# Kernel optimization log

Hardware: AMD Instinct MI355X
Metric: run time of the kernel (lower is better)

The kernel has to match this reference:

```python
import jax, jax.numpy as jnp
import numpy as np


def setup_inputs() -> dict:
    key = jax.random.key(0)
    k1, k2 = jax.random.split(key)
    P, N, D = 8, 4096, 1024
    LOAD = 16384
    data = jax.random.normal(k1, (P, N, D), dtype=jnp.float32)
    tags = jax.random.randint(k2, (P, N), 0, LOAD, dtype=jnp.int64)
    return {"data": data, "tags": tags, "load": LOAD}


def reference(data, tags, load):
    # CombineSF (sparse=False, reduction='add'):
    # concat all path flows along token dim, then scatter-add each token's
    # row into a zeros buffer of shape [load, *route_shape] at its tag index.
    P, N, D = data.shape
    flat_data = data.reshape(P * N, D)          # torch.cat(in_flows_data, dim=0)
    flat_tags = tags.reshape(P * N)             # torch.cat(in_flows_tag, dim=0)
    # zeros(load, D).scatter_(0, tag_indices, data, reduce='add') == segment_sum
    out = jax.ops.segment_sum(flat_data, flat_tags, num_segments=load)
    return out
```

## Files before the change

kernel.cpp:

```cpp
#include <hip/hip_runtime.h>


#define CAP 32
#define DDIM 1024

typedef __attribute__((ext_vector_type(4))) float f4;
typedef __attribute__((ext_vector_type(4))) int i4;

__global__ void hist_fill(const int* __restrict__ tags, int n_rows,
                          int* __restrict__ counts,
                          unsigned short* __restrict__ slots) {
    int r = blockIdx.x * blockDim.x + threadIdx.x;
    if (r < n_rows) {
        int t = tags[r];
        int pos = atomicAdd(&counts[t], 1);
        if (pos < CAP) slots[(long)t * CAP + pos] = (unsigned short)r;
    }
}

__global__ void gather_sum(const float* __restrict__ data,
                           const int* __restrict__ tags,
                           const int* __restrict__ counts,
                           const unsigned short* __restrict__ slots,
                           float* __restrict__ out,
                           int n_rows) {
    int s = blockIdx.x;
    int col = threadIdx.x * 4;
    int k = counts[s];
    f4 acc = {0.f, 0.f, 0.f, 0.f};

    if (k <= CAP) {
        const i4* sp = reinterpret_cast<const i4*>(slots + (long)s * CAP);
        int done = 0;
        #pragma unroll
        for (int w = 0; w < 4; ++w) {
            if (done >= k) break;
            i4 word = sp[w];
            #pragma unroll
            for (int e = 0; e < 4; ++e) {
                int pair = word[e];
                int r0 = pair & 0xFFFF;
                int r1 = (pair >> 16) & 0xFFFF;
                if (done < k) {
                    acc += *reinterpret_cast<const f4*>(data + (long)r0 * DDIM + col);
                    ++done;
                }
                if (done < k) {
                    acc += *reinterpret_cast<const f4*>(data + (long)r1 * DDIM + col);
                    ++done;
                }
            }
        }
    } else {
        for (int r = 0; r < n_rows; ++r) {
            if (tags[r] == s) {
                acc += *reinterpret_cast<const f4*>(data + (long)r * DDIM + col);
            }
        }
    }
    __builtin_nontemporal_store(acc, reinterpret_cast<f4*>(out + (long)s * DDIM + col));
}

__global__ void combine_scatter_add(const float* __restrict__ data,
                                    const int* __restrict__ tags,
                                    float* __restrict__ out,
                                    long total_elems) {
    long stride = (long)gridDim.x * blockDim.x * 4L;
    for (long i = ((long)blockIdx.x * blockDim.x + threadIdx.x) * 4L;
         i < total_elems; i += stride) {
        float4 v = *reinterpret_cast<const float4*>(data + i);
        long row = i >> 10;
        int col = (int)(i & 1023);
        int tag = tags[row];
        float* dst = out + ((long)tag << 10) + col;
        atomicAdd(dst + 0, v.x);
        atomicAdd(dst + 1, v.y);
        atomicAdd(dst + 2, v.z);
        atomicAdd(dst + 3, v.w);
    }
}

extern "C" void kernel_launch(void* const* d_in, const int* in_sizes, int n_in,
                              void* d_out, int out_size, void* d_ws, size_t ws_size,
                              hipStream_t stream) {
    const float* data = (const float*)d_in[0];
    const int* tags = (const int*)d_in[1];
    float* out = (float*)d_out;

    long total = (long)in_sizes[0];
    int n_rows = in_sizes[1];
    int n_seg = out_size / DDIM;

    size_t counts_bytes = (size_t)n_seg * sizeof(int);
    size_t slots_bytes = (size_t)n_seg * CAP * sizeof(unsigned short);
    size_t need = counts_bytes + slots_bytes;

    if (ws_size < need) {
        hipMemsetAsync(d_out, 0, (size_t)out_size * sizeof(float), stream);
        combine_scatter_add<<<2048, 256, 0, stream>>>(data, tags, out, total);
        return;
    }

    int* counts = (int*)d_ws;
    unsigned short* slots = (unsigned short*)((char*)d_ws + counts_bytes);

    hipMemsetAsync(counts, 0, counts_bytes, stream);

    hist_fill<<<(n_rows + 255) / 256, 256, 0, stream>>>(tags, n_rows, counts, slots);

    gather_sum<<<n_seg, 256, 0, stream>>>(data, tags, counts, slots, out, n_rows);
}
```

Baseline: 43.05 us.

## Merge histogram zeroing and fill into one cooperative kernel with packed records

Replaces the memset plus histogram-fill pair with a single cooperative kernel that zeroes the per-segment headers, synchronises the grid, and fills the slots, which removes one launch. Counts and slot indices now sit together in one 64-byte record per segment, so the gather kernel reads its count and the first six indices in a single vector load. A fast path handles segments with six or fewer rows. Slot capacity drops from 32 to 30, so segments with more rows take the slow full scan, and a grid sync over only 128 blocks limits the histogram's parallelism.

```diff
diff --git a/kernel.cpp b/kernel.cpp
--- a/kernel.cpp
+++ b/kernel.cpp
@@ -1,61 +1,94 @@
 #include <hip/hip_runtime.h>
+#include <hip/hip_cooperative_groups.h>
+
+namespace cg = cooperative_groups;
 
 
-#define CAP 32
+#define CAP 30
 #define DDIM 1024
+#define RECB 64
 
 typedef __attribute__((ext_vector_type(4))) float f4;
 typedef __attribute__((ext_vector_type(4))) int i4;
 
+__device__ __forceinline__ void acc_pair(const float* __restrict__ data,
+                                         int pair, int base, int k, int col,
+                                         f4& acc) {
+    int r0 = pair & 0xFFFF;
+    int r1 = (pair >> 16) & 0xFFFF;
+    if (base < k)
+        acc += *reinterpret_cast<const f4*>(data + (long)r0 * DDIM + col);
+    if (base + 1 < k)
+        acc += *reinterpret_cast<const f4*>(data + (long)r1 * DDIM + col);
+}
+
+__global__ void zero_hist(const int* __restrict__ tags, int n_rows, int n_seg,
+                          char* __restrict__ recs) {
+    cg::grid_group grid = cg::this_grid();
+    int tid = blockIdx.x * blockDim.x + threadIdx.x;
+    int nth = gridDim.x * blockDim.x;
+
+    for (int s = tid; s < n_seg; s += nth)
+        *reinterpret_cast<int*>(recs + (long)s * RECB) = 0;
+    grid.sync();
+
+    for (int r = tid; r < n_rows; r += nth) {
+        int t = tags[r];
+        int* hdr = reinterpret_cast<int*>(recs + (long)t * RECB);
+        int pos = atomicAdd(hdr, 1);
+        if (pos < CAP)
+            reinterpret_cast<unsigned short*>(hdr)[2 + pos] = (unsigned short)r;
+    }
+}
+
+__global__ void zero_hdrs(char* __restrict__ recs, int n_seg) {
+    int s = blockIdx.x * blockDim.x + threadIdx.x;
+    if (s < n_seg) *reinterpret_cast<int*>(recs + (long)s * RECB) = 0;
+}
 __global__ void hist_fill(const int* __restrict__ tags, int n_rows,
-                          int* __restrict__ counts,
-                          unsigned short* __restrict__ slots) {
+                          char* __restrict__ recs) {
     int r = blockIdx.x * blockDim.x + threadIdx.x;
     if (r < n_rows) {
         int t = tags[r];
-        int pos = atomicAdd(&counts[t], 1);
-        if (pos < CAP) slots[(long)t * CAP + pos] = (unsigned short)r;
+        int* hdr = reinterpret_cast<int*>(recs + (long)t * RECB);
+        int pos = atomicAdd(hdr, 1);
+        if (pos < CAP)
+            reinterpret_cast<unsigned short*>(hdr)[2 + pos] = (unsigned short)r;
     }
 }
 
 __global__ void gather_sum(const float* __restrict__ data,
                            const int* __restrict__ tags,
-                           const int* __restrict__ counts,
-                           const unsigned short* __restrict__ slots,
+                           const char* __restrict__ recs,
                            float* __restrict__ out,
                            int n_rows) {
     int s = blockIdx.x;
     int col = threadIdx.x * 4;
-    int k = counts[s];
+
+    const i4* rec = reinterpret_cast<const i4*>(recs + (long)s * RECB);
+    i4 w0 = rec[0];
+    int k = w0[0];
+
     f4 acc = {0.f, 0.f, 0.f, 0.f};
-
-    if (k <= CAP) {
-        const i4* sp = reinterpret_cast<const i4*>(slots + (long)s * CAP);
-        int done = 0;
+    if (k <= 6) {
+        acc_pair(data, w0[1], 0, k, col, acc);
+        acc_pair(data, w0[2], 2, k, col, acc);
+        acc_pair(data, w0[3], 4, k, col, acc);
+    } else if (k <= CAP) {
+        acc_pair(data, w0[1], 0, k, col, acc);
+        acc_pair(data, w0[2], 2, k, col, acc);
+        acc_pair(data, w0[3], 4, k, col, acc);
+        i4 w1 = rec[1], w2 = rec[2], w3 = rec[3];
         #pragma unroll
-        for (int w = 0; w < 4; ++w) {
-            if (done >= k) break;
-            i4 word = sp[w];
-            #pragma unroll
-            for (int e = 0; e < 4; ++e) {
-                int pair = word[e];
-                int r0 = pair & 0xFFFF;
-                int r1 = (pair >> 16) & 0xFFFF;
-                if (done < k) {
-                    acc += *reinterpret_cast<const f4*>(data + (long)r0 * DDIM + col);
-                    ++done;
-                }
-                if (done < k) {
-                    acc += *reinterpret_cast<const f4*>(data + (long)r1 * DDIM + col);
-                    ++done;
-                }
-            }
-        }
+        for (int e = 0; e < 4; ++e) acc_pair(data, w1[e], 6 + 2 * e, k, col, acc);
+        #pragma unroll
+        for (int e = 0; e < 4; ++e) acc_pair(data, w2[e], 14 + 2 * e, k, col, acc);
+        #pragma unroll
+        for (int e = 0; e < 4; ++e) acc_pair(data, w3[e], 22 + 2 * e, k, col, acc);
     } else {
         for (int r = 0; r < n_rows; ++r) {
-            if (tags[r] == s) {
+            if (tags[r] == s)
                 acc += *reinterpret_cast<const f4*>(data + (long)r * DDIM + col);
-            }
         }
     }
     __builtin_nontemporal_store(acc, reinterpret_cast<f4*>(out + (long)s * DDIM + col));
@@ -91,22 +124,24 @@
     int n_rows = in_sizes[1];
     int n_seg = out_size / DDIM;
 
-    size_t counts_bytes = (size_t)n_seg * sizeof(int);
-    size_t slots_bytes = (size_t)n_seg * CAP * sizeof(unsigned short);
-    size_t need = counts_bytes + slots_bytes;
+    size_t recs_bytes = (size_t)n_seg * RECB;
 
-    if (ws_size < need) {
+    if (ws_size < recs_bytes) {
         hipMemsetAsync(d_out, 0, (size_t)out_size * sizeof(float), stream);
         combine_scatter_add<<<2048, 256, 0, stream>>>(data, tags, out, total);
         return;
     }
 
-    int* counts = (int*)d_ws;
-    unsigned short* slots = (unsigned short*)((char*)d_ws + counts_bytes);
+    char* recs = (char*)d_ws;
 
-    hipMemsetAsync(counts, 0, counts_bytes, stream);
+    void* args[] = {(void*)&tags, (void*)&n_rows, (void*)&n_seg, (void*)&recs};
+    hipError_t err = hipLaunchCooperativeKernel(
+        reinterpret_cast<const void*>(&zero_hist),
+        dim3(128), dim3(256), args, 0, stream);
+    if (err != hipSuccess) {
+        zero_hdrs<<<(n_seg + 255) / 256, 256, 0, stream>>>(recs, n_seg);
+        hist_fill<<<(n_rows + 255) / 256, 256, 0, stream>>>(tags, n_rows, recs);
+    }
 
-    hist_fill<<<(n_rows + 255) / 256, 256, 0, stream>>>(tags, n_rows, counts, slots);
-
-    gather_sum<<<n_seg, 256, 0, stream>>>(data, tags, counts, slots, out, n_rows);
+    gather_sum<<<n_seg, 256, 0, stream>>>(data, tags, recs, out, n_rows);
 }
```

Result: slower. 66.84 us (+55.3%).
